# Kernel tuning notes

Hardware: AMD Instinct MI355X
Metric: run time of the kernel (lower is better)

Reference implementation:

```python
import jax, jax.numpy as jnp
import numpy as np

N_NODES = 20000
N_EDGES = 160000
F_IN = 512
HIDDEN = 512
N_CLASSES = 40


def setup_inputs() -> dict:
    key = jax.random.key(0)
    k1, k2, k3, k4 = jax.random.split(key, 4)
    x = jax.random.normal(k1, (N_NODES, F_IN), dtype=jnp.float32)
    edge_index = jax.random.randint(k2, (2, N_EDGES), 0, N_NODES, dtype=jnp.int64)
    # Glorot-ish init scale for the linear weights
    W1 = jax.random.normal(k3, (F_IN, HIDDEN), dtype=jnp.float32) / np.sqrt(F_IN)
    b1 = jnp.zeros((HIDDEN,), dtype=jnp.float32)
    W2 = jax.random.normal(k4, (HIDDEN, N_CLASSES), dtype=jnp.float32) / np.sqrt(HIDDEN)
    b2 = jnp.zeros((N_CLASSES,), dtype=jnp.float32)
    return {"x": x, "edge_index": edge_index, "W1": W1, "b1": b1, "W2": W2, "b2": b2}


def _gcn_conv(x, W, b, src, dst, n_nodes):
    """PyG GCNConv: h = D^-1/2 (A+I) D^-1/2 (x W) + b, self-loops already in src/dst."""
    h = x @ W  # [N, out]
    deg = jax.ops.segment_sum(jnp.ones_like(dst, dtype=h.dtype), dst, num_segments=n_nodes)
    deg_inv_sqrt = jnp.where(deg > 0, jax.lax.rsqrt(jnp.maximum(deg, 1.0)), 0.0)
    norm = deg_inv_sqrt[src] * deg_inv_sqrt[dst]  # [E]
    msg = h[src] * norm[:, None]  # [E, out]
    return jax.ops.segment_sum(msg, dst, num_segments=n_nodes) + b


def reference(x, edge_index, W1, b1, W2, b2):
    n = x.shape[0]
    loop = jnp.arange(n, dtype=edge_index.dtype)
    src = jnp.concatenate([edge_index[0], loop])  # add self-loops
    dst = jnp.concatenate([edge_index[1], loop])
    h = _gcn_conv(x, W1, b1, src, dst, n)
    h = jax.nn.relu(h)
    # dropout(p=0.5) is identity in eval mode
    out = _gcn_conv(h, W2, b2, src, dst, n)
    return out
```

## Files before the change

kernel.cpp:

```cpp
#include <hip/hip_runtime.h>
#include <hip/hip_bf16.h>
#include <stdint.h>

#define N_NODES  20000
#define N_EDGES  160000
#define N_CLS    40
#define M_PAD    20096
#define CNT_PAD  20480
#define CAP      64

typedef __bf16 bf16;
typedef __attribute__((ext_vector_type(8))) __bf16 bf16x8;
typedef __attribute__((ext_vector_type(4))) float floatx4;

__device__ inline floatx4 zero4() { floatx4 z = {0.f, 0.f, 0.f, 0.f}; return z; }

typedef __attribute__((address_space(3))) uint32_t lds_u32;
typedef __attribute__((address_space(1))) const uint32_t glb_u32;
__device__ inline void ldst16(const void* g, void* l) {
    __builtin_amdgcn_global_load_lds((glb_u32*)g, (lds_u32*)l, 16, 0, 0);
}

struct Params {
    const float* x; const int* ei; const float* W1; const float* b1;
    const float* W2; const float* b2; float* out;
    bf16 *xb, *w1t, *w2p, *h1; float* h2;
    int *cnt, *colb;
};

#define S0_ZERO 20
#define S0_CONV 5024
#define S0_W1T  128
#define S0_W2P  96
#define S0_TOT  (S0_ZERO + S0_CONV + S0_W1T + S0_W2P)
#define NB_G1   640
#define NB_FILL 625

__global__ __launch_bounds__(256) void k_s0(Params p) {
    const int vb = blockIdx.x, tid = threadIdx.x;
    if (vb < S0_ZERO) {
        int4* dz = (int4*)(p.cnt) + vb * 256 + tid;
        *dz = make_int4(0, 0, 0, 0);
    } else if (vb < S0_ZERO + S0_CONV) {
        long e0 = ((long)(vb - S0_ZERO) * 256 + tid) * 8;
        int row = (int)(e0 >> 9);
        bf16x8 v;
        if (row < N_NODES) {
            const float4* ptr = (const float4*)(p.x + e0);
            float4 f0 = ptr[0], f1 = ptr[1];
            v[0] = (bf16)f0.x; v[1] = (bf16)f0.y; v[2] = (bf16)f0.z; v[3] = (bf16)f0.w;
            v[4] = (bf16)f1.x; v[5] = (bf16)f1.y; v[6] = (bf16)f1.z; v[7] = (bf16)f1.w;
        } else {
            for (int j = 0; j < 8; ++j) v[j] = (bf16)0.f;
        }
        *(bf16x8*)(p.xb + e0) = v;
    } else if (vb < S0_ZERO + S0_CONV + S0_W1T) {
        int t  = (vb - S0_ZERO - S0_CONV) * 256 + tid;
        int n  = t & 511;
        int k0 = (t >> 9) * 8;
        bf16x8 v;
        for (int j = 0; j < 8; ++j) v[j] = (bf16)p.W1[((k0 + j) << 9) + n];
        *(bf16x8*)(p.w1t + n * 512 + k0) = v;
    } else {
        int t = (vb - S0_ZERO - S0_CONV - S0_W1T) * 256 + tid;
        int j = t & 7; int e = t >> 3;
        int lane = e & 63; e >>= 6;
        int nb = e % 3; int kt = e / 3;
        int k = kt * 32 + (lane >> 4) * 8 + j;
        int n = nb * 16 + (lane & 15);
        float v = (n < N_CLS) ? p.W2[k * N_CLS + n] : 0.f;
        p.w2p[t] = (bf16)v;
    }
}

__global__ __launch_bounds__(256) void k_g1f(Params p) {
    if (blockIdx.x >= NB_G1) {
        int e = (blockIdx.x - NB_G1) * 256 + threadIdx.x;
        if (e < N_EDGES) {
            int d = p.ei[N_EDGES + e];
            int j = atomicAdd(&p.cnt[d], 1);
            if (j < CAP) p.colb[d * CAP + j] = p.ei[e];
        }
        return;
    }
    const int g  = blockIdx.x;
    const int mi = (g >> 5) * 8 + (g & 7);
    const int ni = (g >> 3) & 3;
    if (mi >= 157) return;
    __shared__ bf16 As[3 * 4096];
    __shared__ bf16 Bs[3 * 4096];
    const int tid  = threadIdx.x;
    const int lane = tid & 63;
    const int w    = tid >> 6;
    const int wm   = w >> 1, wn = w & 1;
    const int m0   = mi * 128;
    const int n0   = ni * 128;
    const int fr   = lane & 15, fq = lane >> 4;

    floatx4 acc[4][4];
#pragma unroll
    for (int mb = 0; mb < 4; ++mb)
#pragma unroll
        for (int nb = 0; nb < 4; ++nb) acc[mb][nb] = zero4();

    const int sr = lane >> 2;
    const int sk = (((lane & 3) ^ ((lane >> 3) & 3))) * 8;
    const bf16* Ag = p.xb  + (long)(m0 + w * 32 + sr) * 512 + sk;
    const bf16* Bg = p.w1t + (long)(n0 + w * 32 + sr) * 512 + sk;
    const int wof = w * 1024;

    ldst16(Ag,                 As + wof);
    ldst16(Ag + 16 * 512,      As + wof + 512);
    ldst16(Bg,                 Bs + wof);
    ldst16(Bg + 16 * 512,      Bs + wof + 512);
    ldst16(Ag + 32,            As + 4096 + wof);
    ldst16(Ag + 32 + 16 * 512, As + 4096 + wof + 512);
    ldst16(Bg + 32,            Bs + 4096 + wof);
    ldst16(Bg + 32 + 16 * 512, Bs + 4096 + wof + 512);

    const int fqs = (fq ^ ((fr >> 1) & 3)) * 8;

    for (int kt = 0; kt < 16; ++kt) {
        if (kt < 15) {
            asm volatile("s_waitcnt vmcnt(4)" ::: "memory");
        } else {
            asm volatile("s_waitcnt vmcnt(0)" ::: "memory");
        }
        __builtin_amdgcn_sched_barrier(0);
        __builtin_amdgcn_s_barrier();
        __builtin_amdgcn_sched_barrier(0);
        if (kt < 14) {
            const int bo = ((kt + 2) % 3) * 4096;
            const int k2 = (kt + 2) * 32;
            ldst16(Ag + k2,            As + bo + wof);
            ldst16(Ag + k2 + 16 * 512, As + bo + wof + 512);
            ldst16(Bg + k2,            Bs + bo + wof);
            ldst16(Bg + k2 + 16 * 512, Bs + bo + wof + 512);
        }
        const int co = (kt % 3) * 4096;
        bf16x8 af[4], bfv[4];
#pragma unroll
        for (int mb = 0; mb < 4; ++mb)
            af[mb]  = *(const bf16x8*)(As + co + (wm * 64 + mb * 16 + fr) * 32 + fqs);
#pragma unroll
        for (int nb = 0; nb < 4; ++nb)
            bfv[nb] = *(const bf16x8*)(Bs + co + (wn * 64 + nb * 16 + fr) * 32 + fqs);
#pragma unroll
        for (int mb = 0; mb < 4; ++mb)
#pragma unroll
            for (int nb = 0; nb < 4; ++nb)
                acc[mb][nb] = __builtin_amdgcn_mfma_f32_16x16x32_bf16(af[mb], bfv[nb], acc[mb][nb], 0, 0, 0);
    }
#pragma unroll
    for (int mb = 0; mb < 4; ++mb)
#pragma unroll
        for (int nb = 0; nb < 4; ++nb) {
            int row0 = m0 + wm * 64 + mb * 16 + fq * 4;
            int c    = n0 + wn * 64 + nb * 16 + fr;
#pragma unroll
            for (int r = 0; r < 4; ++r)
                p.h1[(long)(row0 + r) * 512 + c] = (bf16)acc[mb][nb][r];
        }
}

__global__ __launch_bounds__(256) void k_agg1g2(Params p) {
    __shared__ bf16 t[16 * 512];
    const int tid = threadIdx.x, l = tid & 63, w = tid >> 6;
    const int ib = blockIdx.x * 16;

    const float4* bp = (const float4*)(p.b1 + l * 8);
    float4 c0 = bp[0], c1 = bp[1];
    float bb[8] = {c0.x, c0.y, c0.z, c0.w, c1.x, c1.y, c1.z, c1.w};

    for (int q4 = 0; q4 < 4; ++q4) {
        const int r = w * 4 + q4;
        const int i = ib + r;
        bf16x8 o;
        if (i >= N_NODES) {
            for (int j = 0; j < 8; ++j) o[j] = (bf16)0.f;
        } else {
            const int ci = p.cnt[i];
            const float di = rsqrtf((float)(ci + 1));
            float acc[8];
            {
                bf16x8 v = *(const bf16x8*)(p.h1 + (long)i * 512 + l * 8);
                const float wi = di * di;
                for (int j = 0; j < 8; ++j) acc[j] = (float)v[j] * wi;
            }
            const int e1 = ci < CAP ? ci : CAP;
            const int* rowcol = p.colb + (long)i * CAP;
            int e = 0;
            for (; e + 8 <= e1; e += 8) {
                int4 sa = *(const int4*)(rowcol + e);
                int4 sb = *(const int4*)(rowcol + e + 4);
                float wgt[8];
                wgt[0] = rsqrtf((float)(p.cnt[sa.x] + 1)) * di;
                wgt[1] = rsqrtf((float)(p.cnt[sa.y] + 1)) * di;
                wgt[2] = rsqrtf((float)(p.cnt[sa.z] + 1)) * di;
                wgt[3] = rsqrtf((float)(p.cnt[sa.w] + 1)) * di;
                wgt[4] = rsqrtf((float)(p.cnt[sb.x] + 1)) * di;
                wgt[5] = rsqrtf((float)(p.cnt[sb.y] + 1)) * di;
                wgt[6] = rsqrtf((float)(p.cnt[sb.z] + 1)) * di;
                wgt[7] = rsqrtf((float)(p.cnt[sb.w] + 1)) * di;
                bf16x8 u[8];
                u[0] = *(const bf16x8*)(p.h1 + (long)sa.x * 512 + l * 8);
                u[1] = *(const bf16x8*)(p.h1 + (long)sa.y * 512 + l * 8);
                u[2] = *(const bf16x8*)(p.h1 + (long)sa.z * 512 + l * 8);
                u[3] = *(const bf16x8*)(p.h1 + (long)sa.w * 512 + l * 8);
                u[4] = *(const bf16x8*)(p.h1 + (long)sb.x * 512 + l * 8);
                u[5] = *(const bf16x8*)(p.h1 + (long)sb.y * 512 + l * 8);
                u[6] = *(const bf16x8*)(p.h1 + (long)sb.z * 512 + l * 8);
                u[7] = *(const bf16x8*)(p.h1 + (long)sb.w * 512 + l * 8);
                for (int q = 0; q < 8; ++q)
                    for (int j = 0; j < 8; ++j) acc[j] += (float)u[q][j] * wgt[q];
            }
            for (; e + 4 <= e1; e += 4) {
                int4 ss = *(const int4*)(rowcol + e);
                float w0 = rsqrtf((float)(p.cnt[ss.x] + 1)) * di;
                float w1 = rsqrtf((float)(p.cnt[ss.y] + 1)) * di;
                float w2 = rsqrtf((float)(p.cnt[ss.z] + 1)) * di;
                float w3 = rsqrtf((float)(p.cnt[ss.w] + 1)) * di;
                bf16x8 u0 = *(const bf16x8*)(p.h1 + (long)ss.x * 512 + l * 8);
                bf16x8 u1 = *(const bf16x8*)(p.h1 + (long)ss.y * 512 + l * 8);
                bf16x8 u2 = *(const bf16x8*)(p.h1 + (long)ss.z * 512 + l * 8);
                bf16x8 u3 = *(const bf16x8*)(p.h1 + (long)ss.w * 512 + l * 8);
                for (int j = 0; j < 8; ++j)
                    acc[j] += (float)u0[j] * w0 + (float)u1[j] * w1 + (float)u2[j] * w2 + (float)u3[j] * w3;
            }
            for (; e < e1; ++e) {
                int s = rowcol[e];
                float wt = rsqrtf((float)(p.cnt[s] + 1)) * di;
                bf16x8 u = *(const bf16x8*)(p.h1 + (long)s * 512 + l * 8);
                for (int j = 0; j < 8; ++j) acc[j] += (float)u[j] * wt;
            }
            for (int j = 0; j < 8; ++j) {
                float f = acc[j] + bb[j];
                f = f > 0.f ? f : 0.f;
                o[j] = (bf16)f;
            }
        }
        *(bf16x8*)((char*)t + r * 1024 + ((l * 16) ^ ((r & 7) << 4))) = o;
    }
    __syncthreads();
    if (w < 3) {
        const int fr = l & 15, fq = l >> 4;
        const int nb = w;
        floatx4 acc2 = zero4();
        for (int kt = 0; kt < 16; ++kt) {
            bf16x8 af = *(const bf16x8*)((const char*)t + fr * 1024 +
                                         ((kt * 64 + fq * 16) ^ ((fr & 7) << 4)));
            bf16x8 bfr = *(const bf16x8*)(p.w2p + ((kt * 3 + nb) * 64 + l) * 8);
            acc2 = __builtin_amdgcn_mfma_f32_16x16x32_bf16(af, bfr, acc2, 0, 0, 0);
        }
        for (int r2 = 0; r2 < 4; ++r2)
            p.h2[(long)(ib + fq * 4 + r2) * 48 + nb * 16 + fr] = acc2[r2];
    }
}

__global__ __launch_bounds__(256) void k_agg2(Params p) {
    const int i = blockIdx.x * 4 + (threadIdx.x >> 6);
    const int l = threadIdx.x & 63;
    if (i >= N_NODES || l >= N_CLS) return;
    const int ci = p.cnt[i];
    const float di = rsqrtf((float)(ci + 1));
    float acc = p.h2[(long)i * 48 + l] * di * di;
    const int e1 = ci < CAP ? ci : CAP;
    const int* rowcol = p.colb + (long)i * CAP;
    int e = 0;
    for (; e + 4 <= e1; e += 4) {
        int4 ss = *(const int4*)(rowcol + e);
        acc += p.h2[(long)ss.x * 48 + l] * (rsqrtf((float)(p.cnt[ss.x] + 1)) * di)
             + p.h2[(long)ss.y * 48 + l] * (rsqrtf((float)(p.cnt[ss.y] + 1)) * di)
             + p.h2[(long)ss.z * 48 + l] * (rsqrtf((float)(p.cnt[ss.z] + 1)) * di)
             + p.h2[(long)ss.w * 48 + l] * (rsqrtf((float)(p.cnt[ss.w] + 1)) * di);
    }
    for (; e < e1; ++e) {
        int s = rowcol[e];
        acc += p.h2[(long)s * 48 + l] * (rsqrtf((float)(p.cnt[s] + 1)) * di);
    }
    p.out[(long)i * N_CLS + l] = acc + p.b2[l];
}


extern "C" void kernel_launch(void* const* d_in, const int* in_sizes, int n_in,
                              void* d_out, int out_size, void* d_ws, size_t ws_size,
                              hipStream_t stream) {
    Params p;
    p.x  = (const float*)d_in[0];
    p.ei = (const int*)d_in[1];
    p.W1 = (const float*)d_in[2];
    p.b1 = (const float*)d_in[3];
    p.W2 = (const float*)d_in[4];
    p.b2 = (const float*)d_in[5];
    p.out = (float*)d_out;

    char* base = (char*)d_ws;
    size_t o = 0;
    auto alloc = [&](size_t bytes) { size_t r = o; o = (o + bytes + 255) & ~(size_t)255; return r; };
    p.xb   = (bf16*)(base + alloc((size_t)M_PAD * 512 * 2));
    p.w1t  = (bf16*)(base + alloc((size_t)512 * 512 * 2));
    p.w2p  = (bf16*)(base + alloc((size_t)24576 * 2));
    p.h1   = (bf16*)(base + alloc((size_t)M_PAD * 512 * 2));
    p.h2   = (float*)(base + alloc((size_t)M_PAD * 48 * 4));
    p.cnt  = (int*)(base + alloc((size_t)CNT_PAD * 4));
    p.colb = (int*)(base + alloc((size_t)N_NODES * CAP * 4));

    k_s0    <<<S0_TOT,           256, 0, stream>>>(p);
    k_g1f   <<<NB_G1 + NB_FILL,  256, 0, stream>>>(p);
    k_agg1g2<<<M_PAD / 16,       256, 0, stream>>>(p);
    k_agg2  <<<N_NODES / 4,      256, 0, stream>>>(p);
}
```

Before: 154.6 us.

## Shrink GEMM1 to single-wave 64x64 tiles with double buffering and no block barrier

Restructures the first GEMM from 256-thread blocks computing 128x128 tiles with a triple-buffered LDS pipeline into 64-thread single-wave blocks computing 64x64 tiles with double buffering. Each wave loads its own tiles, so the per-iteration s_barrier is dropped and only waitcnt is used. The grid grows about fourfold, and the edge-fill tail is retiled to 64 threads. The cost is less data reuse per tile, so more global and LDS traffic goes to the same MFMA work, and the double buffer gives a shorter prefetch distance.

```diff
diff --git a/kernel.cpp b/kernel.cpp
--- a/kernel.cpp
+++ b/kernel.cpp
@@ -33,8 +33,8 @@
 #define S0_W1T  128
 #define S0_W2P  96
 #define S0_TOT  (S0_ZERO + S0_CONV + S0_W1T + S0_W2P)
-#define NB_G1   640
-#define NB_FILL 625
+#define NB_G1   2512
+#define NB_FILL 2500
 
 __global__ __launch_bounds__(256) void k_s0(Params p) {
     const int vb = blockIdx.x, tid = threadIdx.x;
@@ -73,9 +73,9 @@
     }
 }
 
-__global__ __launch_bounds__(256) void k_g1f(Params p) {
+__global__ __launch_bounds__(64) void k_g1f(Params p) {
     if (blockIdx.x >= NB_G1) {
-        int e = (blockIdx.x - NB_G1) * 256 + threadIdx.x;
+        int e = (blockIdx.x - NB_G1) * 64 + threadIdx.x;
         if (e < N_EDGES) {
             int d = p.ei[N_EDGES + e];
             int j = atomicAdd(&p.cnt[d], 1);
@@ -84,17 +84,13 @@
         return;
     }
     const int g  = blockIdx.x;
-    const int mi = (g >> 5) * 8 + (g & 7);
-    const int ni = (g >> 3) & 3;
-    if (mi >= 157) return;
-    __shared__ bf16 As[3 * 4096];
-    __shared__ bf16 Bs[3 * 4096];
-    const int tid  = threadIdx.x;
-    const int lane = tid & 63;
-    const int w    = tid >> 6;
-    const int wm   = w >> 1, wn = w & 1;
-    const int m0   = mi * 128;
-    const int n0   = ni * 128;
+    const int mi = g >> 3;
+    const int ni = g & 7;
+    __shared__ bf16 As[2][64 * 32];
+    __shared__ bf16 Bs[2][64 * 32];
+    const int lane = threadIdx.x;
+    const int m0   = mi * 64;
+    const int n0   = ni * 64;
     const int fr   = lane & 15, fq = lane >> 4;
 
     floatx4 acc[4][4];
@@ -105,58 +101,55 @@
 
     const int sr = lane >> 2;
     const int sk = (((lane & 3) ^ ((lane >> 3) & 3))) * 8;
-    const bf16* Ag = p.xb  + (long)(m0 + w * 32 + sr) * 512 + sk;
-    const bf16* Bg = p.w1t + (long)(n0 + w * 32 + sr) * 512 + sk;
-    const int wof = w * 1024;
-
-    ldst16(Ag,                 As + wof);
-    ldst16(Ag + 16 * 512,      As + wof + 512);
-    ldst16(Bg,                 Bs + wof);
-    ldst16(Bg + 16 * 512,      Bs + wof + 512);
-    ldst16(Ag + 32,            As + 4096 + wof);
-    ldst16(Ag + 32 + 16 * 512, As + 4096 + wof + 512);
-    ldst16(Bg + 32,            Bs + 4096 + wof);
-    ldst16(Bg + 32 + 16 * 512, Bs + 4096 + wof + 512);
+    const bf16* Ag = p.xb  + (long)(m0 + sr) * 512 + sk;
+    const bf16* Bg = p.w1t + (long)(n0 + sr) * 512 + sk;
+
+#define STAGE(b, kk) do { const int ko_ = (kk) * 32;                 \
+        ldst16(Ag + ko_,            As[b]);                          \
+        ldst16(Ag + ko_ + 16 * 512, As[b] + 512);                    \
+        ldst16(Ag + ko_ + 32 * 512, As[b] + 1024);                   \
+        ldst16(Ag + ko_ + 48 * 512, As[b] + 1536);                   \
+        ldst16(Bg + ko_,            Bs[b]);                          \
+        ldst16(Bg + ko_ + 16 * 512, Bs[b] + 512);                    \
+        ldst16(Bg + ko_ + 32 * 512, Bs[b] + 1024);                   \
+        ldst16(Bg + ko_ + 48 * 512, Bs[b] + 1536); } while (0)
+
+    STAGE(0, 0);
+    STAGE(1, 1);
 
     const int fqs = (fq ^ ((fr >> 1) & 3)) * 8;
 
     for (int kt = 0; kt < 16; ++kt) {
+        const int cur = kt & 1;
         if (kt < 15) {
-            asm volatile("s_waitcnt vmcnt(4)" ::: "memory");
+            asm volatile("s_waitcnt vmcnt(8)" ::: "memory");
         } else {
             asm volatile("s_waitcnt vmcnt(0)" ::: "memory");
         }
         __builtin_amdgcn_sched_barrier(0);
-        __builtin_amdgcn_s_barrier();
+        bf16x8 af[4], bfv[4];
+#pragma unroll
+        for (int mb = 0; mb < 4; ++mb)
+            af[mb]  = *(const bf16x8*)(As[cur] + mb * 512 + fr * 32 + fqs);
+#pragma unroll
+        for (int nb = 0; nb < 4; ++nb)
+            bfv[nb] = *(const bf16x8*)(Bs[cur] + nb * 512 + fr * 32 + fqs);
+        asm volatile("s_waitcnt lgkmcnt(0)" ::: "memory");
         __builtin_amdgcn_sched_barrier(0);
-        if (kt < 14) {
-            const int bo = ((kt + 2) % 3) * 4096;
-            const int k2 = (kt + 2) * 32;
-            ldst16(Ag + k2,            As + bo + wof);
-            ldst16(Ag + k2 + 16 * 512, As + bo + wof + 512);
-            ldst16(Bg + k2,            Bs + bo + wof);
-            ldst16(Bg + k2 + 16 * 512, Bs + bo + wof + 512);
-        }
-        const int co = (kt % 3) * 4096;
-        bf16x8 af[4], bfv[4];
-#pragma unroll
-        for (int mb = 0; mb < 4; ++mb)
-            af[mb]  = *(const bf16x8*)(As + co + (wm * 64 + mb * 16 + fr) * 32 + fqs);
-#pragma unroll
-        for (int nb = 0; nb < 4; ++nb)
-            bfv[nb] = *(const bf16x8*)(Bs + co + (wn * 64 + nb * 16 + fr) * 32 + fqs);
+        if (kt < 14) STAGE(cur, kt + 2);
 #pragma unroll
         for (int mb = 0; mb < 4; ++mb)
 #pragma unroll
             for (int nb = 0; nb < 4; ++nb)
                 acc[mb][nb] = __builtin_amdgcn_mfma_f32_16x16x32_bf16(af[mb], bfv[nb], acc[mb][nb], 0, 0, 0);
     }
+#undef STAGE
 #pragma unroll
     for (int mb = 0; mb < 4; ++mb)
 #pragma unroll
         for (int nb = 0; nb < 4; ++nb) {
-            int row0 = m0 + wm * 64 + mb * 16 + fq * 4;
-            int c    = n0 + wn * 64 + nb * 16 + fr;
+            int row0 = m0 + mb * 16 + fq * 4;
+            int c    = n0 + nb * 16 + fr;
 #pragma unroll
             for (int r = 0; r < 4; ++r)
                 p.h1[(long)(row0 + r) * 512 + c] = (bf16)acc[mb][nb][r];
@@ -306,7 +299,7 @@
     p.colb = (int*)(base + alloc((size_t)N_NODES * CAP * 4));
 
     k_s0    <<<S0_TOT,           256, 0, stream>>>(p);
-    k_g1f   <<<NB_G1 + NB_FILL,  256, 0, stream>>>(p);
+    k_g1f   <<<NB_G1 + NB_FILL,  64,  0, stream>>>(p);
     k_agg1g2<<<M_PAD / 16,       256, 0, stream>>>(p);
     k_agg2  <<<N_NODES / 4,      256, 0, stream>>>(p);
 }
```

After: 170.3 us. 1.1x slower.
